# Kernel tuning notes

Measured on AMD Instinct MI355X. Metric: run time of the kernel, lower is better.

Reference implementation:

```python
import jax, jax.numpy as jnp
import numpy as np

B, L, D, H = 4, 2048, 1024, 16
HD = D // H
SCALE = 1.0 / (D / H) ** 0.5


def setup_inputs() -> dict:
    key = jax.random.key(0)
    ks = jax.random.split(key, 11)
    s = 1.0 / np.sqrt(D)
    return {
        "q": jax.random.normal(ks[0], (B, L, D), jnp.float32),
        "k": jax.random.normal(ks[1], (B, L, D), jnp.float32),
        "v": jax.random.normal(ks[2], (B, L, D), jnp.float32),
        "Wq": jax.random.normal(ks[3], (D, D), jnp.float32) * s,
        "bq": jnp.zeros((D,), jnp.float32),
        "Wk": jax.random.normal(ks[4], (D, D), jnp.float32) * s,
        "bk": jnp.zeros((D,), jnp.float32),
        "Wv": jax.random.normal(ks[5], (D, D), jnp.float32) * s,
        "bv": jnp.zeros((D,), jnp.float32),
        "Wo": jax.random.normal(ks[6], (D, D), jnp.float32) * s,
        "bo": jnp.zeros((D,), jnp.float32),
    }


def _split_heads(x):
    # [b, l, h*d] -> [b, h, l, d]
    b, l, _ = x.shape
    return x.reshape(b, l, H, HD).transpose(0, 2, 1, 3)


def reference(q, k, v, Wq, bq, Wk, bk, Wv, bv, Wo, bo):
    # Linear projections (torch Linear: x @ W.T + b)
    qh = _split_heads(q @ Wq.T + bq)            # [b, h, l, d]
    kh = _split_heads(k @ Wk.T + bk)            # [b, h, l, d]
    vh = _split_heads(v @ Wv.T + bv)            # [b, h, l, d]
    scores = jnp.einsum('bhqd,bhkd->bhqk', qh, kh) * SCALE
    attn = jax.nn.softmax(scores, axis=-1)       # dropout p=0 -> identity
    out = jnp.einsum('bhqk,bhkd->bhqd', attn, vh)
    out = out.transpose(0, 2, 1, 3).reshape(q.shape[0], q.shape[1], D)
    return out @ Wo.T + bo
```

## Files before the change

kernel.cpp:

```cpp
#include <hip/hip_runtime.h>


#define Bsz 4
#define Lq 2048
#define Dm 1024
#define NH 16
#define HD 64
#define QSCALE 0.18033688011112042f

typedef unsigned short u16;
typedef __attribute__((ext_vector_type(4))) short bf16x4;
typedef __attribute__((ext_vector_type(8))) short short8;
typedef __attribute__((ext_vector_type(4))) float f32x4;

__device__ __forceinline__ f32x4 mfma16(bf16x4 a, bf16x4 b, f32x4 c) {
#if defined(__HIP_DEVICE_COMPILE__)
  return __builtin_amdgcn_mfma_f32_16x16x16bf16_1k(a, b, c, 0, 0, 0);
#else
  return c;
#endif
}
#define MFMA32(a, b, c) __builtin_amdgcn_mfma_f32_16x16x32_bf16(a, b, c, 0, 0, 0)

typedef __attribute__((address_space(3))) unsigned su32;
typedef __attribute__((address_space(1))) unsigned gu32;
__device__ __forceinline__ void gl_lds16(const u16* g, u16* l) {
  __builtin_amdgcn_global_load_lds((gu32*)(g), (su32*)(l), 16, 0, 0);
}

__device__ __forceinline__ u16 f2b(float x) {
  unsigned u = __builtin_bit_cast(unsigned, x);
  return (u16)((u + 0x7fffu + ((u >> 16) & 1u)) >> 16);
}
__device__ __forceinline__ unsigned pk2(float a, float b) {
  return (unsigned)f2b(a) | ((unsigned)f2b(b) << 16);
}
__device__ __forceinline__ bf16x4 pack4(float a, float b, float c, float d) {
  unsigned lo = __builtin_amdgcn_perm(__builtin_bit_cast(unsigned, b) + 0x8000u,
                                      __builtin_bit_cast(unsigned, a) + 0x8000u, 0x07060302u);
  unsigned hi = __builtin_amdgcn_perm(__builtin_bit_cast(unsigned, d) + 0x8000u,
                                      __builtin_bit_cast(unsigned, c) + 0x8000u, 0x07060302u);
  uint2 u; u.x = lo; u.y = hi;
  return __builtin_bit_cast(bf16x4, u);
}
__device__ __forceinline__ float fexp2(float x) {
#if __has_builtin(__builtin_amdgcn_exp2f)
  return __builtin_amdgcn_exp2f(x);
#else
  return exp2f(x);
#endif
}

__global__ void castk3(const float* __restrict__ q, const float* __restrict__ k,
                       const float* __restrict__ v, u16* __restrict__ dst) {
  const float* s = blockIdx.y == 0 ? q : (blockIdx.y == 1 ? k : v);
  u16* d = dst + (size_t)blockIdx.y * (Bsz * Lq * Dm);
  int i = (blockIdx.x * 256 + threadIdx.x) * 8;
  float4 a = *(const float4*)(s + i);
  float4 b = *(const float4*)(s + i + 4);
  short8 o;
  o[0] = (short)f2b(a.x); o[1] = (short)f2b(a.y);
  o[2] = (short)f2b(a.z); o[3] = (short)f2b(a.w);
  o[4] = (short)f2b(b.x); o[5] = (short)f2b(b.y);
  o[6] = (short)f2b(b.z); o[7] = (short)f2b(b.w);
  *(short8*)(d + i) = o;
}

__global__ void castw(const float* __restrict__ s0, const float* __restrict__ s1,
                      const float* __restrict__ s2, const float* __restrict__ s3,
                      u16* __restrict__ d0, u16* __restrict__ d1,
                      u16* __restrict__ d2, u16* __restrict__ d3) {
  const float* s; u16* d; float sc = 1.0f;
  switch (blockIdx.y) {
    case 0: s = s0; d = d0; sc = QSCALE; break;
    case 1: s = s1; d = d1; break;
    case 2: s = s2; d = d2; break;
    default: s = s3; d = d3; break;
  }
  int i = (blockIdx.x * 256 + threadIdx.x) * 8;
  float4 a = *(const float4*)(s + i);
  float4 b = *(const float4*)(s + i + 4);
  short8 o;
  o[0] = (short)f2b(a.x * sc); o[1] = (short)f2b(a.y * sc);
  o[2] = (short)f2b(a.z * sc); o[3] = (short)f2b(a.w * sc);
  o[4] = (short)f2b(b.x * sc); o[5] = (short)f2b(b.y * sc);
  o[6] = (short)f2b(b.z * sc); o[7] = (short)f2b(b.w * sc);
  *(short8*)(d + i) = o;
}

__global__ __launch_bounds__(256) void qkv_gemm(
    const u16* __restrict__ Ab,
    const u16* __restrict__ Wqb, const u16* __restrict__ Wkb, const u16* __restrict__ Wvb,
    const float* __restrict__ bq, const float* __restrict__ bk, const float* __restrict__ bv,
    u16* __restrict__ Qh, u16* __restrict__ Kh, u16* __restrict__ Vtg)
{
  __shared__ __align__(16) u16 As[128 * 32];
  __shared__ __align__(16) u16 Bs[128 * 32];
  const int z = blockIdx.z;
  const u16* A  = Ab + (size_t)z * (Bsz * Lq * Dm);
  const u16* Bt = z == 0 ? Wqb : (z == 1 ? Wkb : Wvb);
  const float* bias = z == 0 ? bq : (z == 1 ? bk : bv);
  const float bscale = z == 0 ? QSCALE : 1.0f;

  const int tid  = threadIdx.x;
  const int lane = tid & 63;
  const int wave = tid >> 6;
  const int quad = lane >> 4;
  const int r16  = lane & 15;
  const int wm   = (wave >> 1) * 64;
  const int wn   = (wave & 1) * 64;
  const int m0   = blockIdx.y * 128;
  const int n0   = blockIdx.x * 128;

  const u16* ga = A  + (size_t)(m0 + wave * 32 + (lane >> 2)) * Dm + (lane & 3) * 8;
  const u16* gb = Bt + (size_t)(n0 + wave * 32 + (lane >> 2)) * Dm + (lane & 3) * 8;
  u16* la = As + wave * 1024;
  u16* lb = Bs + wave * 1024;

  f32x4 acc[4][4] = {};

  for (int k0 = 0; k0 < Dm; k0 += 32) {
    gl_lds16(ga + k0, la);
    gl_lds16(ga + k0 + 16 * Dm, la + 512);
    gl_lds16(gb + k0, lb);
    gl_lds16(gb + k0 + 16 * Dm, lb + 512);
    __syncthreads();

    short8 af[4], bfr[4];
#pragma unroll
    for (int mt = 0; mt < 4; ++mt) af[mt]  = *(const short8*)&As[(wm + mt * 16 + r16) * 32 + quad * 8];
#pragma unroll
    for (int nt = 0; nt < 4; ++nt) bfr[nt] = *(const short8*)&Bs[(wn + nt * 16 + r16) * 32 + quad * 8];
#pragma unroll
    for (int mt = 0; mt < 4; ++mt)
#pragma unroll
      for (int nt = 0; nt < 4; ++nt)
        acc[mt][nt] = MFMA32(af[mt], bfr[nt], acc[mt][nt]);
    __syncthreads();
  }

#pragma unroll
  for (int mt = 0; mt < 4; ++mt) {
#pragma unroll
    for (int nt = 0; nt < 4; ++nt) {
      int n = n0 + wn + nt * 16 + r16;
      float bv_ = bias[n] * bscale;
      if (z == 2) {
        int m_base = m0 + wm + mt * 16 + quad * 4;
        int b = m_base >> 11, l0 = m_base & 2047;
        int h = n >> 6, d = n & 63;
        u16* dst = Vtg + (((size_t)(b * NH + h)) * HD + d) * Lq + l0;
        uint2 pkd;
        pkd.x = pk2(acc[mt][nt][0] + bv_, acc[mt][nt][1] + bv_);
        pkd.y = pk2(acc[mt][nt][2] + bv_, acc[mt][nt][3] + bv_);
        *(uint2*)dst = pkd;
      } else {
        u16* dst = z == 0 ? Qh : Kh;
#pragma unroll
        for (int j = 0; j < 4; ++j) {
          int m = m0 + wm + mt * 16 + quad * 4 + j;
          int b = m >> 11, l = m & 2047;
          int h = n >> 6,  d = n & 63;
          dst[(((size_t)(b * NH + h)) * Lq + l) * HD + d] = f2b(acc[mt][nt][j] + bv_);
        }
      }
    }
  }
}

__global__ __launch_bounds__(256) void gemm_wo(
    const u16* __restrict__ A, const u16* __restrict__ Bt,
    const float* __restrict__ bias, float* __restrict__ C)
{
  __shared__ __align__(16) u16 As[128 * 32];
  __shared__ __align__(16) u16 Bs[64 * 32];
  const int tid  = threadIdx.x;
  const int lane = tid & 63;
  const int wave = tid >> 6;
  const int quad = lane >> 4;
  const int r16  = lane & 15;
  const int wm   = wave * 32;
  const int m0   = blockIdx.y * 128;
  const int n0   = blockIdx.x * 64;

  const u16* ga = A  + (size_t)(m0 + wave * 32 + (lane >> 2)) * Dm + (lane & 3) * 8;
  const u16* gb = Bt + (size_t)(n0 + wave * 16 + (lane >> 2)) * Dm + (lane & 3) * 8;
  u16* la = As + wave * 1024;
  u16* lb = Bs + wave * 512;

  f32x4 acc[2][4] = {};

  for (int k0 = 0; k0 < Dm; k0 += 32) {
    gl_lds16(ga + k0, la);
    gl_lds16(ga + k0 + 16 * Dm, la + 512);
    gl_lds16(gb + k0, lb);
    __syncthreads();

    short8 af[2], bfr[4];
#pragma unroll
    for (int mt = 0; mt < 2; ++mt) af[mt]  = *(const short8*)&As[(wm + mt * 16 + r16) * 32 + quad * 8];
#pragma unroll
    for (int nt = 0; nt < 4; ++nt) bfr[nt] = *(const short8*)&Bs[(nt * 16 + r16) * 32 + quad * 8];
#pragma unroll
    for (int mt = 0; mt < 2; ++mt)
#pragma unroll
      for (int nt = 0; nt < 4; ++nt)
        acc[mt][nt] = MFMA32(af[mt], bfr[nt], acc[mt][nt]);
    __syncthreads();
  }

#pragma unroll
  for (int mt = 0; mt < 2; ++mt) {
#pragma unroll
    for (int nt = 0; nt < 4; ++nt) {
      int n = n0 + nt * 16 + r16;
      float bv = bias[n];
#pragma unroll
      for (int j = 0; j < 4; ++j) {
        int m = m0 + wm + mt * 16 + quad * 4 + j;
        C[(size_t)m * Dm + n] = acc[mt][nt][j] + bv;
      }
    }
  }
}

__global__ __launch_bounds__(256) void attn3(
    const u16* __restrict__ Qh, const u16* __restrict__ Kh,
    const u16* __restrict__ Vtg, u16* __restrict__ Oa)
{
  const int bh = blockIdx.y;
  const int qt = blockIdx.x;
  const int tid = threadIdx.x, lane = tid & 63, wave = tid >> 6;
  const int quad = lane >> 4, r16 = lane & 15;

  __shared__ __align__(16) u16 Ks[64][72];
  __shared__ __align__(16) u16 Vt[64][72];

  const int qbase = qt * 128 + wave * 32;
  short8 aq[2][2];
#pragma unroll
  for (int qf = 0; qf < 2; ++qf) {
    const size_t qrow = ((size_t)bh * Lq + qbase + qf * 16 + r16) * HD;
    aq[qf][0] = *(const short8*)(Qh + qrow + quad * 8);
    aq[qf][1] = *(const short8*)(Qh + qrow + 32 + quad * 8);
  }

  f32x4 oacc[2][4] = {};
  float lsum[2] = {0.f, 0.f};

  const int srow = tid >> 2;
  const int scid = (tid & 3) * 16;
  const u16* kg = Kh  + ((size_t)bh * Lq + srow) * HD + scid;
  const u16* vg = Vtg + ((size_t)bh * HD + srow) * Lq + scid;

  short8 pk0 = *(const short8*)(kg);
  short8 pk1 = *(const short8*)(kg + 8);
  short8 pv0 = *(const short8*)(vg);
  short8 pv1 = *(const short8*)(vg + 8);

  for (int t = 0; t < 32; ++t) {
    __syncthreads();
    *(short8*)&Ks[srow][scid]     = pk0;
    *(short8*)&Ks[srow][scid + 8] = pk1;
    *(short8*)&Vt[srow][scid]     = pv0;
    *(short8*)&Vt[srow][scid + 8] = pv1;
    __syncthreads();
    if (t < 31) {
      const u16* kgn = kg + (size_t)(t + 1) * 64 * HD;
      const u16* vgn = vg + (t + 1) * 64;
      pk0 = *(const short8*)(kgn);
      pk1 = *(const short8*)(kgn + 8);
      pv0 = *(const short8*)(vgn);
      pv1 = *(const short8*)(vgn + 8);
    }

#pragma unroll
    for (int mt = 0; mt < 4; ++mt) {
      short8 kf0 = *(const short8*)&Ks[mt * 16 + r16][quad * 8];
      short8 kf1 = *(const short8*)&Ks[mt * 16 + r16][32 + quad * 8];
      bf16x4 vf[4];
#pragma unroll
      for (int nt = 0; nt < 4; ++nt)
        vf[nt] = *(const bf16x4*)&Vt[nt * 16 + r16][mt * 16 + quad * 4];
#pragma unroll
      for (int qf = 0; qf < 2; ++qf) {
        f32x4 z = {};
        z = MFMA32(kf0, aq[qf][0], z);
        z = MFMA32(kf1, aq[qf][1], z);
        float p0 = fexp2(z[0]);
        float p1 = fexp2(z[1]);
        float p2 = fexp2(z[2]);
        float p3 = fexp2(z[3]);
        lsum[qf] += (p0 + p1) + (p2 + p3);
        bf16x4 pb = pack4(p0, p1, p2, p3);
#pragma unroll
        for (int nt = 0; nt < 4; ++nt)
          oacc[qf][nt] = mfma16(vf[nt], pb, oacc[qf][nt]);
      }
    }
  }

  const int b = bh >> 4, h = bh & 15;
  float linv[2];
#pragma unroll
  for (int qf = 0; qf < 2; ++qf) {
    float r = lsum[qf];
    r += __shfl_xor(r, 16);
    r += __shfl_xor(r, 32);
    linv[qf] = 1.0f / r;
  }
#pragma unroll
  for (int qf = 0; qf < 2; ++qf) {
    int q = qbase + qf * 16 + r16;
    size_t rowb = ((size_t)(b * Lq + q)) * Dm + h * HD;
#pragma unroll
    for (int nt = 0; nt < 4; ++nt) {
      f32x4 o = oacc[qf][nt];
      uint2 pkd;
      pkd.x = pk2(o[0] * linv[qf], o[1] * linv[qf]);
      pkd.y = pk2(o[2] * linv[qf], o[3] * linv[qf]);
      *(uint2*)&Oa[rowb + nt * 16 + quad * 4] = pkd;
    }
  }
}

extern "C" void kernel_launch(void* const* d_in, const int* in_sizes, int n_in,
                              void* d_out, int out_size, void* d_ws, size_t ws_size,
                              hipStream_t stream) {
  const float* q  = (const float*)d_in[0];
  const float* k  = (const float*)d_in[1];
  const float* v  = (const float*)d_in[2];
  const float* Wq = (const float*)d_in[3];
  const float* bq = (const float*)d_in[4];
  const float* Wk = (const float*)d_in[5];
  const float* bk = (const float*)d_in[6];
  const float* Wv = (const float*)d_in[7];
  const float* bv = (const float*)d_in[8];
  const float* Wo = (const float*)d_in[9];
  const float* bo = (const float*)d_in[10];

  const int NA = Bsz * Lq * Dm;
  u16* abuf = (u16*)d_ws;
  u16* Qh   = abuf + (size_t)3 * NA;
  u16* Kh   = Qh   + NA;
  u16* Vtg  = Kh   + NA;
  u16* wqb  = Vtg  + NA;
  u16* wkb  = wqb  + 1048576;
  u16* wvb  = wkb  + 1048576;
  u16* wob  = wvb  + 1048576;

  castw<<<dim3(512, 4), 256, 0, stream>>>(Wq, Wk, Wv, Wo, wqb, wkb, wvb, wob);
  castk3<<<dim3(NA / 2048, 3), 256, 0, stream>>>(q, k, v, abuf);

  qkv_gemm<<<dim3(8, 64, 3), 256, 0, stream>>>(abuf, wqb, wkb, wvb, bq, bk, bv, Qh, Kh, Vtg);

  attn3<<<dim3(Lq / 128, Bsz * NH), 256, 0, stream>>>(Qh, Kh, Vtg, abuf);

  gemm_wo<<<dim3(16, 64), 256, 0, stream>>>(abuf, wob, bo, (float*)d_out);
}
```

Baseline: 371.6 us.

## Use 16x16x32 MFMA for PV product with permuted V layout

The attention P·V product moves from 16x16x16 bf16 MFMAs to 16x16x32 MFMAs by grouping two score tiles per step, so each P fragment packs eight probabilities. To match the operand lane mapping, the QKV GEMM epilogue writes transposed V with a permuted sequence index within each 32-element block. This halves the PV MFMA count and widens V LDS reads. The cost is higher register pressure from holding two score tiles at once, plus coupling between the V write layout and the attention kernel.

```diff
diff --git a/kernel.cpp b/kernel.cpp
--- a/kernel.cpp
+++ b/kernel.cpp
@@ -13,13 +13,6 @@
 typedef __attribute__((ext_vector_type(8))) short short8;
 typedef __attribute__((ext_vector_type(4))) float f32x4;
 
-__device__ __forceinline__ f32x4 mfma16(bf16x4 a, bf16x4 b, f32x4 c) {
-#if defined(__HIP_DEVICE_COMPILE__)
-  return __builtin_amdgcn_mfma_f32_16x16x16bf16_1k(a, b, c, 0, 0, 0);
-#else
-  return c;
-#endif
-}
 #define MFMA32(a, b, c) __builtin_amdgcn_mfma_f32_16x16x32_bf16(a, b, c, 0, 0, 0)
 
 typedef __attribute__((address_space(3))) unsigned su32;
@@ -35,13 +28,9 @@
 __device__ __forceinline__ unsigned pk2(float a, float b) {
   return (unsigned)f2b(a) | ((unsigned)f2b(b) << 16);
 }
-__device__ __forceinline__ bf16x4 pack4(float a, float b, float c, float d) {
-  unsigned lo = __builtin_amdgcn_perm(__builtin_bit_cast(unsigned, b) + 0x8000u,
-                                      __builtin_bit_cast(unsigned, a) + 0x8000u, 0x07060302u);
-  unsigned hi = __builtin_amdgcn_perm(__builtin_bit_cast(unsigned, d) + 0x8000u,
-                                      __builtin_bit_cast(unsigned, c) + 0x8000u, 0x07060302u);
-  uint2 u; u.x = lo; u.y = hi;
-  return __builtin_bit_cast(bf16x4, u);
+__device__ __forceinline__ unsigned pk2p(float a, float b) {
+  return __builtin_amdgcn_perm(__builtin_bit_cast(unsigned, b) + 0x8000u,
+                               __builtin_bit_cast(unsigned, a) + 0x8000u, 0x07060302u);
 }
 __device__ __forceinline__ float fexp2(float x) {
 #if __has_builtin(__builtin_amdgcn_exp2f)
@@ -148,8 +137,9 @@
       if (z == 2) {
         int m_base = m0 + wm + mt * 16 + quad * 4;
         int b = m_base >> 11, l0 = m_base & 2047;
+        int lp = (l0 & ~31) | (((l0 >> 2) & 3) << 3) | (((l0 >> 4) & 1) << 2);
         int h = n >> 6, d = n & 63;
-        u16* dst = Vtg + (((size_t)(b * NH + h)) * HD + d) * Lq + l0;
+        u16* dst = Vtg + (((size_t)(b * NH + h)) * HD + d) * Lq + lp;
         uint2 pkd;
         pkd.x = pk2(acc[mt][nt][0] + bv_, acc[mt][nt][1] + bv_);
         pkd.y = pk2(acc[mt][nt][2] + bv_, acc[mt][nt][3] + bv_);
@@ -224,7 +214,7 @@
   }
 }
 
-__global__ __launch_bounds__(256) void attn3(
+__global__ __launch_bounds__(256) void attn4(
     const u16* __restrict__ Qh, const u16* __restrict__ Kh,
     const u16* __restrict__ Vtg, u16* __restrict__ Oa)
 {
@@ -275,27 +265,40 @@
     }
 
 #pragma unroll
-    for (int mt = 0; mt < 4; ++mt) {
-      short8 kf0 = *(const short8*)&Ks[mt * 16 + r16][quad * 8];
-      short8 kf1 = *(const short8*)&Ks[mt * 16 + r16][32 + quad * 8];
-      bf16x4 vf[4];
+    for (int ks = 0; ks < 2; ++ks) {
+      f32x4 stq[2][2];
+#pragma unroll
+      for (int mtl = 0; mtl < 2; ++mtl) {
+        const int mt = 2 * ks + mtl;
+        short8 kf0 = *(const short8*)&Ks[mt * 16 + r16][quad * 8];
+        short8 kf1 = *(const short8*)&Ks[mt * 16 + r16][32 + quad * 8];
+#pragma unroll
+        for (int qf = 0; qf < 2; ++qf) {
+          f32x4 zz = {};
+          zz = MFMA32(kf0, aq[qf][0], zz);
+          zz = MFMA32(kf1, aq[qf][1], zz);
+          stq[qf][mtl] = zz;
+        }
+      }
+      short8 vf[4];
 #pragma unroll
       for (int nt = 0; nt < 4; ++nt)
-        vf[nt] = *(const bf16x4*)&Vt[nt * 16 + r16][mt * 16 + quad * 4];
+        vf[nt] = *(const short8*)&Vt[nt * 16 + r16][ks * 32 + quad * 8];
 #pragma unroll
       for (int qf = 0; qf < 2; ++qf) {
-        f32x4 z = {};
-        z = MFMA32(kf0, aq[qf][0], z);
-        z = MFMA32(kf1, aq[qf][1], z);
-        float p0 = fexp2(z[0]);
-        float p1 = fexp2(z[1]);
-        float p2 = fexp2(z[2]);
-        float p3 = fexp2(z[3]);
-        lsum[qf] += (p0 + p1) + (p2 + p3);
-        bf16x4 pb = pack4(p0, p1, p2, p3);
+        f32x4 sa = stq[qf][0], sb = stq[qf][1];
+        float p0 = fexp2(sa[0]), p1 = fexp2(sa[1]), p2 = fexp2(sa[2]), p3 = fexp2(sa[3]);
+        float p4 = fexp2(sb[0]), p5 = fexp2(sb[1]), p6 = fexp2(sb[2]), p7 = fexp2(sb[3]);
+        lsum[qf] += ((p0 + p1) + (p2 + p3)) + ((p4 + p5) + (p6 + p7));
+        uint4 pu;
+        pu.x = pk2p(p0, p1);
+        pu.y = pk2p(p2, p3);
+        pu.z = pk2p(p4, p5);
+        pu.w = pk2p(p6, p7);
+        short8 pb = __builtin_bit_cast(short8, pu);
 #pragma unroll
         for (int nt = 0; nt < 4; ++nt)
-          oacc[qf][nt] = mfma16(vf[nt], pb, oacc[qf][nt]);
+          oacc[qf][nt] = MFMA32(vf[nt], pb, oacc[qf][nt]);
       }
     }
   }
@@ -354,7 +357,7 @@
 
   qkv_gemm<<<dim3(8, 64, 3), 256, 0, stream>>>(abuf, wqb, wkb, wvb, bq, bk, bv, Qh, Kh, Vtg);
 
-  attn3<<<dim3(Lq / 128, Bsz * NH), 256, 0, stream>>>(Qh, Kh, Vtg, abuf);
+  attn4<<<dim3(Lq / 128, Bsz * NH), 256, 0, stream>>>(Qh, Kh, Vtg, abuf);
 
   gemm_wo<<<dim3(16, 64), 256, 0, stream>>>(abuf, wob, bo, (float*)d_out);
 }
```

New measurement: 365.9 us. Within noise of the previous version (-1.5%).
